# Performance work log

Measured on AMD Instinct MI355X. Metric: run time of the kernel, lower is better.

## Reference

```python
import jax, jax.numpy as jnp
import numpy as np

TOPK = 8
N_EXPERTS = 64
ROUTE_SCALE = 1.0


def setup_inputs() -> dict:
    key = jax.random.key(0)
    k1, k2 = jax.random.split(key)
    x = jax.random.normal(k1, (16, 256, 64, 64), dtype=jnp.float32)
    gate_w = jax.random.normal(k2, (64, 256, 3, 3), dtype=jnp.float32) * 0.02  # [E, C, kh, kw]
    bias = jnp.zeros((64,), dtype=jnp.float32)  # load-balancing bias buffer
    return {"x": x, "gate_w": gate_w, "bias": bias}


def reference(x, gate_w, bias):
    # 3x3 conv, stride 1, pad 1 (SAME), no conv bias -> expert logits [B, E, H, W]
    logits = jax.lax.conv_general_dilated(
        x, gate_w, window_strides=(1, 1), padding="SAME",
        dimension_numbers=("NCHW", "OIHW", "NCHW"))
    scores = jax.nn.sigmoid(logits)                 # [B, E, H, W]
    s = jnp.moveaxis(scores, 1, -1)                 # [B, H, W, E]
    biased = s + bias                               # bias broadcast over experts
    _, idx = jax.lax.top_k(biased, TOPK)            # [B, H, W, K] (topk on biased scores)
    w = jnp.take_along_axis(s, idx, axis=-1)        # gather UNbiased scores
    w = jax.nn.softmax(w, axis=-1) * ROUTE_SCALE    # softmax over the K selected experts
    weights = jnp.moveaxis(w, -1, 1)                # [B, K, H, W] to match torch layout
    indices = jnp.moveaxis(idx, -1, 1)              # [B, K, H, W]
    counts = jnp.zeros((N_EXPERTS,), jnp.int32).at[idx.ravel()].add(1)  # bincount
    return weights, indices, counts
```

## Files before the change

### kernel.cpp

```cpp
#include <hip/hip_runtime.h>


typedef _Float16 half8 __attribute__((ext_vector_type(8)));
typedef __attribute__((ext_vector_type(4))) float f32x4;

#define LOG2E 1.44269504f

__device__ __forceinline__ unsigned short f2h_bits(float f) {
    _Float16 h = (_Float16)f;
    unsigned short b;
    __builtin_memcpy(&b, &h, 2);
    return b;
}

constexpr int WB_U4 = 8 * 9 * 4 * 64;

__global__ __launch_bounds__(256) void gate_prep(const float* __restrict__ gw,
                                                 unsigned short* __restrict__ wB,
                                                 float* __restrict__ out) {
    int g = blockIdx.x * 256 + threadIdx.x;
    if (blockIdx.x == 0 && threadIdx.x < 64) out[1048576 + threadIdx.x] = 0.f;
    if (g >= WB_U4) return;
    int lane = g & 63;
    int nt   = (g >> 6) & 3;
    int rest = g >> 8;
    int t = rest % 9, q = rest / 9;
    int e  = nt * 16 + (lane & 15);
    int c0 = q * 32 + (lane >> 4) * 8;
    unsigned short o[8];
#pragma unroll
    for (int j = 0; j < 8; ++j)
        o[j] = f2h_bits(gw[(e * 256 + c0 + j) * 9 + t]);
    uint4 pk;
    pk.x = (unsigned)o[0] | ((unsigned)o[1] << 16);
    pk.y = (unsigned)o[2] | ((unsigned)o[3] << 16);
    pk.z = (unsigned)o[4] | ((unsigned)o[5] << 16);
    pk.w = (unsigned)o[6] | ((unsigned)o[7] << 16);
    ((uint4*)wB)[g] = pk;
}

constexpr int CSTR = 40;
constexpr int SLAB = 3 * 66 * CSTR;
constexpr int SSTR = 68;

__global__ __launch_bounds__(256, 4) void gate_main(
    const float* __restrict__ x, const float* __restrict__ bias,
    const unsigned short* __restrict__ wB, float* __restrict__ out) {
    __shared__ unsigned short xs[2 * SLAB];
    __shared__ float bias_s[64];
    __shared__ int   hist[64];

    const int tid  = threadIdx.x;
    const int lane = tid & 63;
    const int rw   = tid >> 6;
    const int blk  = blockIdx.x;
    const int b    = blk & 15;
    const int r    = blk >> 4;

    if (tid < 64) { bias_s[tid] = bias[tid]; hist[tid] = 0; }

    bool tEx[4], tOk[4];
    int  tSrc[4], tDst[4];
#pragma unroll
    for (int i = 0; i < 4; ++i) {
        int T = tid + i * 256;
        tEx[i] = (T < 792);
        int chh = T / 198, s = T - chh * 198;
        int row2 = s / 66, wp = s - row2 * 66;
        int gr = r - 1 + row2, gwc = wp - 1;
        tOk[i]  = tEx[i] && (gr >= 0) && (gr < 64) && (gwc >= 0) && (gwc < 64);
        tSrc[i] = ((b * 256 + chh * 8) * 64 + gr) * 64 + gwc;
        tDst[i] = (row2 * 66 + wp) * CSTR + chh * 8;
    }

    float tb0[8], tb1[8];
    auto issue = [&](int i, int q, float* tb) {
        if (tOk[i]) {
            const float* p = x + tSrc[i] + q * 131072;
#pragma unroll
            for (int u = 0; u < 8; ++u) tb[u] = p[u * 4096];
        } else {
#pragma unroll
            for (int u = 0; u < 8; ++u) tb[u] = 0.f;
        }
    };
    auto commit = [&](int i, const float* tb, unsigned short* dst) {
        if (tEx[i]) {
            uint4 pk;
            pk.x = (unsigned)f2h_bits(tb[0]) | ((unsigned)f2h_bits(tb[1]) << 16);
            pk.y = (unsigned)f2h_bits(tb[2]) | ((unsigned)f2h_bits(tb[3]) << 16);
            pk.z = (unsigned)f2h_bits(tb[4]) | ((unsigned)f2h_bits(tb[5]) << 16);
            pk.w = (unsigned)f2h_bits(tb[6]) | ((unsigned)f2h_bits(tb[7]) << 16);
            *(uint4*)(dst + tDst[i]) = pk;
        }
    };

    const int ph = rw >> 1, eh = rw & 1;
    half8 Aa[3][2];
    uint4 Bb[3][2];
    auto prefA = [&](const unsigned short* buf, int t, int slot) {
        const int kh = t / 3, kw = t % 3;
        const unsigned short* abase =
            buf + (kh * 66 + ph * 32 + (lane & 15) + kw) * CSTR + (lane >> 4) * 8;
#pragma unroll
        for (int mt = 0; mt < 2; ++mt)
            Aa[slot][mt] = *(const half8*)(abase + mt * 16 * CSTR);
    };
    auto prefB = [&](int q, int t, int slot) {
        const uint4* bp = (const uint4*)wB + ((q * 9 + t) * 4 + eh * 2) * 64 + lane;
#pragma unroll
        for (int nt = 0; nt < 2; ++nt) Bb[slot][nt] = bp[nt * 64];
    };

    f32x4 acc[2][2];
#pragma unroll
    for (int mt = 0; mt < 2; ++mt)
#pragma unroll
        for (int nt = 0; nt < 2; ++nt) acc[mt][nt] = (f32x4){0.f, 0.f, 0.f, 0.f};

    auto mfma_tap = [&](int slot) {
#pragma unroll
        for (int nt = 0; nt < 2; ++nt) {
            half8 bfr;
            __builtin_memcpy(&bfr, &Bb[slot][nt], 16);
#pragma unroll
            for (int mt = 0; mt < 2; ++mt)
                acc[mt][nt] = __builtin_amdgcn_mfma_f32_16x16x32_f16(
                    Aa[slot][mt], bfr, acc[mt][nt], 0, 0, 0);
        }
    };

    issue(0, 0, tb0); issue(1, 0, tb1);
    commit(0, tb0, xs); commit(1, tb1, xs);
    issue(2, 0, tb0); issue(3, 0, tb1);
    commit(2, tb0, xs); commit(3, tb1, xs);
    __syncthreads();

#pragma unroll 1
    for (int q = 0; q < 8; ++q) {
        const unsigned short* cur = xs + (q & 1) * SLAB;
        unsigned short*       nxt = xs + ((q + 1) & 1) * SLAB;
        const bool st = (q < 7);
        if (st) { issue(0, q + 1, tb0); issue(1, q + 1, tb1); }
        prefA(cur, 0, 0); prefB(q, 0, 0);
        prefA(cur, 1, 1); prefB(q, 1, 1); mfma_tap(0);
        prefA(cur, 2, 2); prefB(q, 2, 2); mfma_tap(1);
        prefA(cur, 3, 0); prefB(q, 3, 0); mfma_tap(2);
        prefA(cur, 4, 1); prefB(q, 4, 1); mfma_tap(0);
        if (st) {
            commit(0, tb0, nxt); commit(1, tb1, nxt);
            issue(2, q + 1, tb0); issue(3, q + 1, tb1);
        }
        prefA(cur, 5, 2); prefB(q, 5, 2); mfma_tap(1);
        prefA(cur, 6, 0); prefB(q, 6, 0); mfma_tap(2);
        prefA(cur, 7, 1); prefB(q, 7, 1); mfma_tap(0);
        prefA(cur, 8, 2); prefB(q, 8, 2); mfma_tap(1);
        mfma_tap(2);
        if (st) { commit(2, tb0, nxt); commit(3, tb1, nxt); }
        __syncthreads();
    }

    float* scf = (float*)xs;
#pragma unroll
    for (int mt = 0; mt < 2; ++mt)
#pragma unroll
        for (int nt = 0; nt < 2; ++nt)
#pragma unroll
            for (int rr = 0; rr < 4; ++rr) {
                float v = acc[mt][nt][rr];
                float s = 1.f / (1.f + __builtin_amdgcn_exp2f(-v * LOG2E));
                int p = ph * 32 + mt * 16 + ((lane >> 4) << 2) + rr;
                int e = eh * 32 + nt * 16 + (lane & 15);
                scf[p * SSTR + e] = s;
            }
    __syncthreads();

    if (tid < 64) {
        const float* row = scf + tid * SSTR;
        float tv[8];
        int   ti[8];
#pragma unroll
        for (int k = 0; k < 8; ++k) { tv[k] = -3.0e38f; ti[k] = 0; }
#pragma unroll
        for (int j4 = 0; j4 < 16; ++j4) {
            f32x4 blkv = *(const f32x4*)(row + j4 * 4);
#pragma unroll
            for (int j = 0; j < 4; ++j) {
                int   e  = j4 * 4 + j;
                float bs = blkv[j] + bias_s[e];
                if (bs > tv[7]) {
                    tv[7] = bs; ti[7] = e;
#pragma unroll
                    for (int k = 7; k > 0; --k) {
                        float fa = tv[k - 1], fb = tv[k];
                        int   ia = ti[k - 1], ib = ti[k];
                        bool  sw = fb > fa;
                        tv[k - 1] = sw ? fb : fa; tv[k] = sw ? fa : fb;
                        ti[k - 1] = sw ? ib : ia; ti[k] = sw ? ia : ib;
                    }
                }
            }
        }
        float u[8], mx = -3.0e38f;
#pragma unroll
        for (int k = 0; k < 8; ++k) { u[k] = tv[k] - bias_s[ti[k]]; mx = fmaxf(mx, u[k]); }
        float ex[8], sum = 0.f;
#pragma unroll
        for (int k = 0; k < 8; ++k) { ex[k] = __builtin_amdgcn_exp2f((u[k] - mx) * LOG2E); sum += ex[k]; }
        float inv = 1.f / sum;

        int obase = b * 32768 + r * 64 + tid;
#pragma unroll
        for (int k = 0; k < 8; ++k) {
            out[obase + k * 4096]          = ex[k] * inv;
            out[524288 + obase + k * 4096] = (float)ti[k];
            atomicAdd(&hist[ti[k]], 1);
        }
    }
    __syncthreads();
    if (tid < 64) atomicAdd(out + 1048576 + tid, (float)hist[tid]);
}

extern "C" void kernel_launch(void* const* d_in, const int* in_sizes, int n_in,
                              void* d_out, int out_size, void* d_ws, size_t ws_size,
                              hipStream_t stream) {
    const float* x    = (const float*)d_in[0];
    const float* gw   = (const float*)d_in[1];
    const float* bias = (const float*)d_in[2];
    float* out = (float*)d_out;
    unsigned short* wB = (unsigned short*)d_ws;

    gate_prep<<<72, 256, 0, stream>>>(gw, wB, out);
    gate_main<<<1024, 256, 0, stream>>>(x, bias, wB, out);
}
```

Baseline: 153.8 us.

## Deepen global-load prefetch to two stages and pipeline weight fetches across chunks

Restructures the software pipeline of the implicit-GEMM conv loop. Global loads of x are now issued two channel-chunks ahead into four register buffers and committed to LDS at the start of the next iteration. Weight (B) fragment loads are shifted so the next chunk's first taps are prefetched during the current chunk's tail. The LDS buffers are zero-filled once up front so padded halo entries no longer need explicit zero stores, and sched_barriers pin the issue point. This aims to hide global-memory latency more fully, at the cost of more live registers (32 extra floats), which may pressure occupancy at 4 waves/SIMD.

Result: faster. 142.7 us (-7.2%).

```diff
diff --git a/kernel.cpp b/kernel.cpp
--- a/kernel.cpp
+++ b/kernel.cpp
@@ -59,38 +59,45 @@
 
     if (tid < 64) { bias_s[tid] = bias[tid]; hist[tid] = 0; }
 
-    bool tEx[4], tOk[4];
+    {
+        uint4 z = {0u, 0u, 0u, 0u};
+        uint4* p = (uint4*)xs;
+#pragma unroll
+        for (int i = 0; i < 8; ++i) {
+            int idx = tid + i * 256;
+            if (idx < 2 * SLAB / 8) p[idx] = z;
+        }
+    }
+
+    bool tOk[4];
     int  tSrc[4], tDst[4];
 #pragma unroll
     for (int i = 0; i < 4; ++i) {
         int T = tid + i * 256;
-        tEx[i] = (T < 792);
+        bool ex = (T < 792);
         int chh = T / 198, s = T - chh * 198;
         int row2 = s / 66, wp = s - row2 * 66;
         int gr = r - 1 + row2, gwc = wp - 1;
-        tOk[i]  = tEx[i] && (gr >= 0) && (gr < 64) && (gwc >= 0) && (gwc < 64);
+        tOk[i]  = ex && (gr >= 0) && (gr < 64) && (gwc >= 0) && (gwc < 64);
         tSrc[i] = ((b * 256 + chh * 8) * 64 + gr) * 64 + gwc;
         tDst[i] = (row2 * 66 + wp) * CSTR + chh * 8;
     }
 
-    float tb0[8], tb1[8];
-    auto issue = [&](int i, int q, float* tb) {
+    float tb[4][8];
+    auto issueT = [&](int i, int dq) {
         if (tOk[i]) {
-            const float* p = x + tSrc[i] + q * 131072;
-#pragma unroll
-            for (int u = 0; u < 8; ++u) tb[u] = p[u * 4096];
-        } else {
-#pragma unroll
-            for (int u = 0; u < 8; ++u) tb[u] = 0.f;
-        }
-    };
-    auto commit = [&](int i, const float* tb, unsigned short* dst) {
-        if (tEx[i]) {
+            const float* p = x + tSrc[i] + dq * 131072;
+#pragma unroll
+            for (int u = 0; u < 8; ++u) tb[i][u] = p[u * 4096];
+        }
+    };
+    auto commitT = [&](int i, unsigned short* dst) {
+        if (tOk[i]) {
             uint4 pk;
-            pk.x = (unsigned)f2h_bits(tb[0]) | ((unsigned)f2h_bits(tb[1]) << 16);
-            pk.y = (unsigned)f2h_bits(tb[2]) | ((unsigned)f2h_bits(tb[3]) << 16);
-            pk.z = (unsigned)f2h_bits(tb[4]) | ((unsigned)f2h_bits(tb[5]) << 16);
-            pk.w = (unsigned)f2h_bits(tb[6]) | ((unsigned)f2h_bits(tb[7]) << 16);
+            pk.x = (unsigned)f2h_bits(tb[i][0]) | ((unsigned)f2h_bits(tb[i][1]) << 16);
+            pk.y = (unsigned)f2h_bits(tb[i][2]) | ((unsigned)f2h_bits(tb[i][3]) << 16);
+            pk.z = (unsigned)f2h_bits(tb[i][4]) | ((unsigned)f2h_bits(tb[i][5]) << 16);
+            pk.w = (unsigned)f2h_bits(tb[i][6]) | ((unsigned)f2h_bits(tb[i][7]) << 16);
             *(uint4*)(dst + tDst[i]) = pk;
         }
     };
@@ -106,8 +113,8 @@
         for (int mt = 0; mt < 2; ++mt)
             Aa[slot][mt] = *(const half8*)(abase + mt * 16 * CSTR);
     };
-    auto prefB = [&](int q, int t, int slot) {
-        const uint4* bp = (const uint4*)wB + ((q * 9 + t) * 4 + eh * 2) * 64 + lane;
+    auto prefB = [&](int T9, int slot) {
+        const uint4* bp = (const uint4*)wB + (T9 * 4 + eh * 2) * 64 + lane;
 #pragma unroll
         for (int nt = 0; nt < 2; ++nt) Bb[slot][nt] = bp[nt * 64];
     };
@@ -130,33 +137,36 @@
         }
     };
 
-    issue(0, 0, tb0); issue(1, 0, tb1);
-    commit(0, tb0, xs); commit(1, tb1, xs);
-    issue(2, 0, tb0); issue(3, 0, tb1);
-    commit(2, tb0, xs); commit(3, tb1, xs);
+    __syncthreads();
+
+    issueT(0, 0); issueT(1, 0); issueT(2, 0); issueT(3, 0);
+    commitT(0, xs); commitT(1, xs); commitT(2, xs); commitT(3, xs);
+    issueT(0, 1); issueT(1, 1); issueT(2, 1); issueT(3, 1);
+    prefB(0, 0); prefB(1, 1); prefB(2, 2);
     __syncthreads();
 
 #pragma unroll 1
     for (int q = 0; q < 8; ++q) {
         const unsigned short* cur = xs + (q & 1) * SLAB;
         unsigned short*       nxt = xs + ((q + 1) & 1) * SLAB;
-        const bool st = (q < 7);
-        if (st) { issue(0, q + 1, tb0); issue(1, q + 1, tb1); }
-        prefA(cur, 0, 0); prefB(q, 0, 0);
-        prefA(cur, 1, 1); prefB(q, 1, 1); mfma_tap(0);
-        prefA(cur, 2, 2); prefB(q, 2, 2); mfma_tap(1);
-        prefA(cur, 3, 0); prefB(q, 3, 0); mfma_tap(2);
-        prefA(cur, 4, 1); prefB(q, 4, 1); mfma_tap(0);
-        if (st) {
-            commit(0, tb0, nxt); commit(1, tb1, nxt);
-            issue(2, q + 1, tb0); issue(3, q + 1, tb1);
-        }
-        prefA(cur, 5, 2); prefB(q, 5, 2); mfma_tap(1);
-        prefA(cur, 6, 0); prefB(q, 6, 0); mfma_tap(2);
-        prefA(cur, 7, 1); prefB(q, 7, 1); mfma_tap(0);
-        prefA(cur, 8, 2); prefB(q, 8, 2); mfma_tap(1);
-        mfma_tap(2);
-        if (st) { commit(2, tb0, nxt); commit(3, tb1, nxt); }
+        const int  T0  = q * 9;
+        const bool cmt = (q < 7);
+        const bool iss = (q < 6);
+
+        prefA(cur, 0, 0); prefA(cur, 1, 1);
+        if (cmt) { commitT(0, nxt); commitT(1, nxt); commitT(2, nxt); commitT(3, nxt); }
+        mfma_tap(0); prefB(T0 + 3, 0); prefA(cur, 2, 2);
+        mfma_tap(1); prefB(T0 + 4, 1); prefA(cur, 3, 0);
+        mfma_tap(2); prefB(T0 + 5, 2); prefA(cur, 4, 1);
+        mfma_tap(0); prefB(T0 + 6, 0); prefA(cur, 5, 2);
+        mfma_tap(1); prefB(T0 + 7, 1); prefA(cur, 6, 0);
+        mfma_tap(2); prefB(T0 + 8, 2); prefA(cur, 7, 1);
+        __builtin_amdgcn_sched_barrier(0);
+        if (iss) { issueT(0, q + 2); issueT(1, q + 2); issueT(2, q + 2); issueT(3, q + 2); }
+        __builtin_amdgcn_sched_barrier(0);
+        mfma_tap(0); if (cmt) prefB(T0 + 9, 0);  prefA(cur, 8, 2);
+        mfma_tap(1); if (cmt) prefB(T0 + 10, 1);
+        mfma_tap(2); if (cmt) prefB(T0 + 11, 2);
         __syncthreads();
     }
 
```
